# Performance work log

Hardware: AMD Instinct MI355X
Metric: run time of the kernel (lower is better)

The kernel has to match this reference:

```python
import jax, jax.numpy as jnp
import numpy as np

N, K, F = 16384, 64, 2048
ALPHA = 1.0
GAMMA = 1.0


def setup_inputs() -> dict:
    key = jax.random.key(0)
    k1, k2, k3, k4 = jax.random.split(key, 4)
    features = jax.random.normal(k1, (N, F), dtype=jnp.float32)
    idx = jax.random.randint(k2, (N,), 0, K)
    labels = jax.nn.one_hot(idx, K, dtype=jnp.float32)  # [N, K] one-hot
    # original initializes clusters to zeros (degenerate); use small random values
    cluster = jax.random.normal(k3, (K, F), dtype=jnp.float32) * 0.02
    class_weight = jax.random.uniform(k4, (K,), dtype=jnp.float32, minval=0.5, maxval=1.5)
    return {"features": features, "labels": labels, "cluster": cluster,
            "class_weight": class_weight}


def reference(features, labels, cluster, class_weight):
    # ci: cluster center of each sample's argmax label  [N, F]
    idx = jnp.argmax(labels, axis=1)
    ci = cluster[idx]
    # numerator: squared distance to own center  [N]
    nume = jnp.sum((features - ci) ** 2, axis=1)
    # denom: sum_j ||c_j - c_i||^2 + alpha  (TF flattens cj to [N, K*F] and
    # tiles ci K times; the squared norm over that axis is exactly this sum)
    d2 = jnp.sum((cluster[:, None, :] - cluster[None, :, :]) ** 2, axis=-1)  # [K, K]
    row_sum = jnp.sum(d2, axis=1)                                            # [K]
    denom = row_sum[idx] + ALPHA                                             # [N]
    loss = (nume / denom)[:, None]                                           # [N, 1]
    # cluster update: weighted_delta[k,f] = sum_n cw[n,k]*labels[n,k]*(x[n,f]-c[k,f])/denom[n]
    # with cw[n,k] = labels[n,k] * class_weight[k]. Expressed without the
    # [N,K,F] intermediates the TF code materializes:
    A = (labels * labels) * class_weight[None, :] / denom[:, None]  # [N, K]
    weighted_delta = jnp.einsum('nk,nf->kf', A, features) - jnp.sum(A, axis=0)[:, None] * cluster
    new_cluster = cluster - GAMMA * weighted_delta  # assign_sub side effect
    return loss, new_cluster
```

## Files before the change

### kernel.cpp

```cpp
#include <hip/hip_runtime.h>

#define NROWS 16384
#define KC 64
#define FDIM 2048
#define F4 (FDIM / 4)
#define ALPHA 1.0f
#define GAMMA 1.0f
#define ROWS 16
#define HB 128
#define ROWS_PER_HB 128

typedef float f32x4 __attribute__((ext_vector_type(4)));

__global__ __launch_bounds__(256) void k_argmax_hist(
    const float* __restrict__ labels, int* __restrict__ idx,
    int* __restrict__ blockHist, float4* __restrict__ delta4) {
    __shared__ int hist[KC];
    int t = threadIdx.x, w = t >> 6, lane = t & 63;
    if (t < KC) hist[t] = 0;
    float4 z = {0.f, 0.f, 0.f, 0.f};
    delta4[blockIdx.x * 256 + t] = z;
    __syncthreads();
    int rowbase = blockIdx.x * ROWS_PER_HB + w * 32;
    #pragma unroll
    for (int r0 = 0; r0 < 32; r0 += 4) {
        float v0 = labels[(rowbase + r0 + 0) * KC + lane];
        float v1 = labels[(rowbase + r0 + 1) * KC + lane];
        float v2 = labels[(rowbase + r0 + 2) * KC + lane];
        float v3 = labels[(rowbase + r0 + 3) * KC + lane];
        unsigned long long m0 = __ballot(v0 > 0.5f);
        unsigned long long m1 = __ballot(v1 > 0.5f);
        unsigned long long m2 = __ballot(v2 > 0.5f);
        unsigned long long m3 = __ballot(v3 > 0.5f);
        if (lane == 0) {
            int k0 = __ffsll(m0) - 1;
            int k1 = __ffsll(m1) - 1;
            int k2 = __ffsll(m2) - 1;
            int k3 = __ffsll(m3) - 1;
            idx[rowbase + r0 + 0] = k0;
            idx[rowbase + r0 + 1] = k1;
            idx[rowbase + r0 + 2] = k2;
            idx[rowbase + r0 + 3] = k3;
            atomicAdd(&hist[k0], 1);
            atomicAdd(&hist[k1], 1);
            atomicAdd(&hist[k2], 1);
            atomicAdd(&hist[k3], 1);
        }
    }
    __syncthreads();
    if (t < KC) blockHist[blockIdx.x * KC + t] = hist[t];
}

__global__ __launch_bounds__(256) void k_prefix_rowsum(
    const int* __restrict__ blockHist, int* __restrict__ blockBase,
    int* __restrict__ counts, int* __restrict__ offsets,
    const float* __restrict__ cluster, const float* __restrict__ cw,
    float* __restrict__ inv_denom, float* __restrict__ scale) {
    if (blockIdx.x == 0) {
        int t = threadIdx.x, c = t >> 6, k = t & 63;
        __shared__ int chunkTot[4][KC];
        __shared__ int kTot[KC];
        int acc = 0;
        for (int b = c * 32; b < c * 32 + 32; ++b) acc += blockHist[b * KC + k];
        chunkTot[c][k] = acc;
        __syncthreads();
        if (c == 0) {
            int tot = chunkTot[0][k] + chunkTot[1][k] + chunkTot[2][k] + chunkTot[3][k];
            kTot[k] = tot;
            counts[k] = tot;
        }
        __syncthreads();
        if (t == 0) {
            int a = 0;
            for (int j = 0; j < KC; ++j) { offsets[j] = a; a += kTot[j]; }
        }
        int run = 0;
        for (int cc = 0; cc < c; ++cc) run += chunkTot[cc][k];
        for (int b = c * 32; b < c * 32 + 32; ++b) {
            blockBase[b * KC + k] = run;
            run += blockHist[b * KC + k];
        }
    } else {
        int k = blockIdx.x - 1, t = threadIdx.x;
        const float4* c4 = (const float4*)cluster;
        float4 a0 = c4[k * F4 + t];
        float4 a1 = c4[k * F4 + 256 + t];
        float acc = 0.f;
        for (int j = 0; j < KC; ++j) {
            float4 b0 = c4[j * F4 + t];
            float4 b1 = c4[j * F4 + 256 + t];
            float d;
            d = a0.x - b0.x; acc += d * d;
            d = a0.y - b0.y; acc += d * d;
            d = a0.z - b0.z; acc += d * d;
            d = a0.w - b0.w; acc += d * d;
            d = a1.x - b1.x; acc += d * d;
            d = a1.y - b1.y; acc += d * d;
            d = a1.z - b1.z; acc += d * d;
            d = a1.w - b1.w; acc += d * d;
        }
        #pragma unroll
        for (int off = 32; off >= 1; off >>= 1) acc += __shfl_down(acc, off);
        __shared__ float red[4];
        if ((t & 63) == 0) red[t >> 6] = acc;
        __syncthreads();
        if (t == 0) {
            float denom = red[0] + red[1] + red[2] + red[3] + ALPHA;
            inv_denom[k] = 1.0f / denom;
            scale[k]     = cw[k] / denom;
        }
    }
}

__global__ __launch_bounds__(128) void k_scatter(
    const int* __restrict__ idx, const int* __restrict__ offsets,
    const int* __restrict__ blockBase, int* __restrict__ order) {
    __shared__ int cur[KC];
    int t = threadIdx.x;
    if (t < KC) cur[t] = offsets[t] + blockBase[blockIdx.x * KC + t];
    __syncthreads();
    int n = blockIdx.x * ROWS_PER_HB + t;
    int k = idx[n];
    int p = atomicAdd(&cur[k], 1);
    order[p] = n;
}

__global__ __launch_bounds__(256) void k_main(
    const float* __restrict__ features, const float* __restrict__ cluster,
    const int* __restrict__ idx, const int* __restrict__ order,
    const float* __restrict__ inv_denom, float* __restrict__ delta,
    float* __restrict__ lossPart) {
    int t = threadIdx.x;
    int pair = blockIdx.x >> 1, half = blockIdx.x & 1;
    int foff = half * 256;
    __shared__ float part[ROWS][256];
    __shared__ int onum[ROWS];
    __shared__ int okk[ROWS];
    if (t < ROWS) {
        int n = order[pair * ROWS + t];
        onum[t] = n;
        okk[t]  = idx[n];
    }
    __syncthreads();

    const f32x4* f4 = (const f32x4*)features;
    const f32x4* c4 = (const f32x4*)cluster;
    float4 s = {0.f, 0.f, 0.f, 0.f};
    int k0 = okk[0];

    if (okk[ROWS - 1] == k0) {
        f32x4 cv = c4[k0 * F4 + foff + t];
        for (int r = 0; r < ROWS; r += 4) {
            f32x4 x0 = __builtin_nontemporal_load(&f4[(size_t)onum[r + 0] * F4 + foff + t]);
            f32x4 x1 = __builtin_nontemporal_load(&f4[(size_t)onum[r + 1] * F4 + foff + t]);
            f32x4 x2 = __builtin_nontemporal_load(&f4[(size_t)onum[r + 2] * F4 + foff + t]);
            f32x4 x3 = __builtin_nontemporal_load(&f4[(size_t)onum[r + 3] * F4 + foff + t]);
            float d, p;
            s.x += x0.x; s.y += x0.y; s.z += x0.z; s.w += x0.w;
            p = 0.f;
            d = x0.x - cv.x; p += d * d;
            d = x0.y - cv.y; p += d * d;
            d = x0.z - cv.z; p += d * d;
            d = x0.w - cv.w; p += d * d;
            part[r + 0][t] = p;
            s.x += x1.x; s.y += x1.y; s.z += x1.z; s.w += x1.w;
            p = 0.f;
            d = x1.x - cv.x; p += d * d;
            d = x1.y - cv.y; p += d * d;
            d = x1.z - cv.z; p += d * d;
            d = x1.w - cv.w; p += d * d;
            part[r + 1][t] = p;
            s.x += x2.x; s.y += x2.y; s.z += x2.z; s.w += x2.w;
            p = 0.f;
            d = x2.x - cv.x; p += d * d;
            d = x2.y - cv.y; p += d * d;
            d = x2.z - cv.z; p += d * d;
            d = x2.w - cv.w; p += d * d;
            part[r + 2][t] = p;
            s.x += x3.x; s.y += x3.y; s.z += x3.z; s.w += x3.w;
            p = 0.f;
            d = x3.x - cv.x; p += d * d;
            d = x3.y - cv.y; p += d * d;
            d = x3.z - cv.z; p += d * d;
            d = x3.w - cv.w; p += d * d;
            part[r + 3][t] = p;
        }
        float* dk = delta + k0 * FDIM + half * 1024;
        atomicAdd(&dk[t * 4 + 0], s.x);
        atomicAdd(&dk[t * 4 + 1], s.y);
        atomicAdd(&dk[t * 4 + 2], s.z);
        atomicAdd(&dk[t * 4 + 3], s.w);
    } else {
        int cur_k = -1;
        f32x4 cv;
        for (int r = 0; r < ROWS; ++r) {
            int k = okk[r];
            if (k != cur_k) {
                if (cur_k >= 0) {
                    float* dk = delta + cur_k * FDIM + half * 1024;
                    atomicAdd(&dk[t * 4 + 0], s.x);
                    atomicAdd(&dk[t * 4 + 1], s.y);
                    atomicAdd(&dk[t * 4 + 2], s.z);
                    atomicAdd(&dk[t * 4 + 3], s.w);
                    s.x = s.y = s.z = s.w = 0.f;
                }
                cv = c4[k * F4 + foff + t];
                cur_k = k;
            }
            f32x4 x = __builtin_nontemporal_load(&f4[(size_t)onum[r] * F4 + foff + t]);
            s.x += x.x; s.y += x.y; s.z += x.z; s.w += x.w;
            float d, p = 0.f;
            d = x.x - cv.x; p += d * d;
            d = x.y - cv.y; p += d * d;
            d = x.z - cv.z; p += d * d;
            d = x.w - cv.w; p += d * d;
            part[r][t] = p;
        }
        float* dk = delta + cur_k * FDIM + half * 1024;
        atomicAdd(&dk[t * 4 + 0], s.x);
        atomicAdd(&dk[t * 4 + 1], s.y);
        atomicAdd(&dk[t * 4 + 2], s.z);
        atomicAdd(&dk[t * 4 + 3], s.w);
    }
    __syncthreads();
    int w = t >> 6, l = t & 63;
    for (int r = w; r < ROWS; r += 4) {
        float v = part[r][l] + part[r][l + 64] + part[r][l + 128] + part[r][l + 192];
        #pragma unroll
        for (int off = 32; off >= 1; off >>= 1) v += __shfl_down(v, off);
        if (l == 0) {
            lossPart[half * NROWS + onum[r]] = v * inv_denom[okk[r]];
        }
    }
}

__global__ __launch_bounds__(256) void k_finalize(
    const float* __restrict__ cluster, const float* __restrict__ delta,
    const int* __restrict__ counts, const float* __restrict__ scale,
    const float* __restrict__ lossPart, float* __restrict__ outc,
    float* __restrict__ loss) {
    int b = blockIdx.x, t = threadIdx.x;
    if (b < 128) {
        int e = b * 256 + t;
        int k = e >> 9;
        const float4* c4 = (const float4*)cluster;
        const float4* d4 = (const float4*)delta;
        float4 c = c4[e], d = d4[e];
        float s = scale[k], cnt = (float)counts[k];
        float4 o;
        o.x = c.x - GAMMA * s * (d.x - cnt * c.x);
        o.y = c.y - GAMMA * s * (d.y - cnt * c.y);
        o.z = c.z - GAMMA * s * (d.z - cnt * c.z);
        o.w = c.w - GAMMA * s * (d.w - cnt * c.w);
        ((float4*)outc)[e] = o;
    } else {
        int n = (b - 128) * 256 + t;
        loss[n] = lossPart[n] + lossPart[NROWS + n];
    }
}

extern "C" void kernel_launch(void* const* d_in, const int* in_sizes, int n_in,
                              void* d_out, int out_size, void* d_ws, size_t ws_size,
                              hipStream_t stream) {
    const float* features = (const float*)d_in[0];
    const float* labels   = (const float*)d_in[1];
    const float* cluster  = (const float*)d_in[2];
    const float* cw       = (const float*)d_in[3];
    float* loss = (float*)d_out;
    float* outc = (float*)d_out + NROWS;

    char*  ws        = (char*)d_ws;
    float* delta     = (float*)ws;
    int*   counts    = (int*)(ws + (size_t)KC * FDIM * 4);
    int*   offsets   = counts + KC;
    float* inv_denom = (float*)(offsets + KC);
    float* scale     = inv_denom + KC;
    int*   idx       = (int*)(scale + KC);
    int*   order     = idx + NROWS;
    int*   blockHist = order + NROWS;
    int*   blockBase = blockHist + HB * KC;
    float* lossPart  = (float*)(blockBase + HB * KC);

    k_argmax_hist<<<HB, 256, 0, stream>>>(labels, idx, blockHist, (float4*)delta);
    k_prefix_rowsum<<<KC + 1, 256, 0, stream>>>(blockHist, blockBase, counts, offsets,
                                                cluster, cw, inv_denom, scale);
    k_scatter<<<HB, 128, 0, stream>>>(idx, offsets, blockBase, order);
    k_main<<<(NROWS / ROWS) * 2, 256, 0, stream>>>(features, cluster, idx, order,
                                                   inv_denom, delta, lossPart);
    k_finalize<<<192, 256, 0, stream>>>(cluster, delta, counts, scale, lossPart,
                                        outc, loss);
}
```

Before: 225.2 us.

## Merge histogram, prefix and scatter into per-class sort kernel, widen main loads

```diff
diff --git a/kernel.cpp b/kernel.cpp
--- a/kernel.cpp
+++ b/kernel.cpp
@@ -7,21 +7,19 @@
 #define ALPHA 1.0f
 #define GAMMA 1.0f
 #define ROWS 16
-#define HB 128
-#define ROWS_PER_HB 128
+#define AB 128
+#define ROWS_PER_AB 128
+#define MAXCL 640
 
 typedef float f32x4 __attribute__((ext_vector_type(4)));
 
-__global__ __launch_bounds__(256) void k_argmax_hist(
+__global__ __launch_bounds__(256) void k_argmax(
     const float* __restrict__ labels, int* __restrict__ idx,
-    int* __restrict__ blockHist, float4* __restrict__ delta4) {
-    __shared__ int hist[KC];
+    float4* __restrict__ delta4) {
     int t = threadIdx.x, w = t >> 6, lane = t & 63;
-    if (t < KC) hist[t] = 0;
     float4 z = {0.f, 0.f, 0.f, 0.f};
     delta4[blockIdx.x * 256 + t] = z;
-    __syncthreads();
-    int rowbase = blockIdx.x * ROWS_PER_HB + w * 32;
+    int rowbase = blockIdx.x * ROWS_PER_AB + w * 32;
     #pragma unroll
     for (int r0 = 0; r0 < 32; r0 += 4) {
         float v0 = labels[(rowbase + r0 + 0) * KC + lane];
@@ -33,55 +31,45 @@
         unsigned long long m2 = __ballot(v2 > 0.5f);
         unsigned long long m3 = __ballot(v3 > 0.5f);
         if (lane == 0) {
-            int k0 = __ffsll(m0) - 1;
-            int k1 = __ffsll(m1) - 1;
-            int k2 = __ffsll(m2) - 1;
-            int k3 = __ffsll(m3) - 1;
-            idx[rowbase + r0 + 0] = k0;
-            idx[rowbase + r0 + 1] = k1;
-            idx[rowbase + r0 + 2] = k2;
-            idx[rowbase + r0 + 3] = k3;
-            atomicAdd(&hist[k0], 1);
-            atomicAdd(&hist[k1], 1);
-            atomicAdd(&hist[k2], 1);
-            atomicAdd(&hist[k3], 1);
-        }
-    }
-    __syncthreads();
-    if (t < KC) blockHist[blockIdx.x * KC + t] = hist[t];
-}
-
-__global__ __launch_bounds__(256) void k_prefix_rowsum(
-    const int* __restrict__ blockHist, int* __restrict__ blockBase,
-    int* __restrict__ counts, int* __restrict__ offsets,
+            idx[rowbase + r0 + 0] = __ffsll(m0) - 1;
+            idx[rowbase + r0 + 1] = __ffsll(m1) - 1;
+            idx[rowbase + r0 + 2] = __ffsll(m2) - 1;
+            idx[rowbase + r0 + 3] = __ffsll(m3) - 1;
+        }
+    }
+}
+
+__global__ __launch_bounds__(256) void k_sort_rowsum(
+    const int* __restrict__ idx, int* __restrict__ order,
+    int* __restrict__ counts,
     const float* __restrict__ cluster, const float* __restrict__ cw,
     float* __restrict__ inv_denom, float* __restrict__ scale) {
-    if (blockIdx.x == 0) {
-        int t = threadIdx.x, c = t >> 6, k = t & 63;
-        __shared__ int chunkTot[4][KC];
-        __shared__ int kTot[KC];
-        int acc = 0;
-        for (int b = c * 32; b < c * 32 + 32; ++b) acc += blockHist[b * KC + k];
-        chunkTot[c][k] = acc;
+    int t = threadIdx.x;
+    if (blockIdx.x < KC) {
+        int k = blockIdx.x;
+        __shared__ int list[MAXCL];
+        __shared__ int lcnt;
+        __shared__ int redv[4];
+        if (t == 0) lcnt = 0;
         __syncthreads();
-        if (c == 0) {
-            int tot = chunkTot[0][k] + chunkTot[1][k] + chunkTot[2][k] + chunkTot[3][k];
-            kTot[k] = tot;
-            counts[k] = tot;
-        }
+        int myless = 0;
+        #pragma unroll 4
+        for (int i = 0; i < NROWS / 256; ++i) {
+            int n = i * 256 + t;
+            int v = idx[n];
+            myless += (v < k) ? 1 : 0;
+            if (v == k) { int p = atomicAdd(&lcnt, 1); list[p] = n; }
+        }
+        #pragma unroll
+        for (int off = 32; off >= 1; off >>= 1) myless += __shfl_down(myless, off);
+        if ((t & 63) == 0) redv[t >> 6] = myless;
         __syncthreads();
-        if (t == 0) {
-            int a = 0;
-            for (int j = 0; j < KC; ++j) { offsets[j] = a; a += kTot[j]; }
-        }
-        int run = 0;
-        for (int cc = 0; cc < c; ++cc) run += chunkTot[cc][k];
-        for (int b = c * 32; b < c * 32 + 32; ++b) {
-            blockBase[b * KC + k] = run;
-            run += blockHist[b * KC + k];
-        }
+        int offk = redv[0] + redv[1] + redv[2] + redv[3];
+        int cnt = lcnt;
+        if (t == 0) counts[k] = cnt;
+        for (int i = t; i < cnt; i += 256) order[offk + i] = list[i];
     } else {
-        int k = blockIdx.x - 1, t = threadIdx.x;
+        int k = blockIdx.x - KC;
         const float4* c4 = (const float4*)cluster;
         float4 a0 = c4[k * F4 + t];
         float4 a1 = c4[k * F4 + 256 + t];
@@ -112,19 +100,6 @@
     }
 }
 
-__global__ __launch_bounds__(128) void k_scatter(
-    const int* __restrict__ idx, const int* __restrict__ offsets,
-    const int* __restrict__ blockBase, int* __restrict__ order) {
-    __shared__ int cur[KC];
-    int t = threadIdx.x;
-    if (t < KC) cur[t] = offsets[t] + blockBase[blockIdx.x * KC + t];
-    __syncthreads();
-    int n = blockIdx.x * ROWS_PER_HB + t;
-    int k = idx[n];
-    int p = atomicAdd(&cur[k], 1);
-    order[p] = n;
-}
-
 __global__ __launch_bounds__(256) void k_main(
     const float* __restrict__ features, const float* __restrict__ cluster,
     const int* __restrict__ idx, const int* __restrict__ order,
@@ -150,40 +125,21 @@
 
     if (okk[ROWS - 1] == k0) {
         f32x4 cv = c4[k0 * F4 + foff + t];
-        for (int r = 0; r < ROWS; r += 4) {
-            f32x4 x0 = __builtin_nontemporal_load(&f4[(size_t)onum[r + 0] * F4 + foff + t]);
-            f32x4 x1 = __builtin_nontemporal_load(&f4[(size_t)onum[r + 1] * F4 + foff + t]);
-            f32x4 x2 = __builtin_nontemporal_load(&f4[(size_t)onum[r + 2] * F4 + foff + t]);
-            f32x4 x3 = __builtin_nontemporal_load(&f4[(size_t)onum[r + 3] * F4 + foff + t]);
-            float d, p;
-            s.x += x0.x; s.y += x0.y; s.z += x0.z; s.w += x0.w;
-            p = 0.f;
-            d = x0.x - cv.x; p += d * d;
-            d = x0.y - cv.y; p += d * d;
-            d = x0.z - cv.z; p += d * d;
-            d = x0.w - cv.w; p += d * d;
-            part[r + 0][t] = p;
-            s.x += x1.x; s.y += x1.y; s.z += x1.z; s.w += x1.w;
-            p = 0.f;
-            d = x1.x - cv.x; p += d * d;
-            d = x1.y - cv.y; p += d * d;
-            d = x1.z - cv.z; p += d * d;
-            d = x1.w - cv.w; p += d * d;
-            part[r + 1][t] = p;
-            s.x += x2.x; s.y += x2.y; s.z += x2.z; s.w += x2.w;
-            p = 0.f;
-            d = x2.x - cv.x; p += d * d;
-            d = x2.y - cv.y; p += d * d;
-            d = x2.z - cv.z; p += d * d;
-            d = x2.w - cv.w; p += d * d;
-            part[r + 2][t] = p;
-            s.x += x3.x; s.y += x3.y; s.z += x3.z; s.w += x3.w;
-            p = 0.f;
-            d = x3.x - cv.x; p += d * d;
-            d = x3.y - cv.y; p += d * d;
-            d = x3.z - cv.z; p += d * d;
-            d = x3.w - cv.w; p += d * d;
-            part[r + 3][t] = p;
+        for (int r = 0; r < ROWS; r += 8) {
+            f32x4 x[8];
+            #pragma unroll
+            for (int j = 0; j < 8; ++j)
+                x[j] = __builtin_nontemporal_load(&f4[(size_t)onum[r + j] * F4 + foff + t]);
+            #pragma unroll
+            for (int j = 0; j < 8; ++j) {
+                s.x += x[j].x; s.y += x[j].y; s.z += x[j].z; s.w += x[j].w;
+                float d, p = 0.f;
+                d = x[j].x - cv.x; p += d * d;
+                d = x[j].y - cv.y; p += d * d;
+                d = x[j].z - cv.z; p += d * d;
+                d = x[j].w - cv.w; p += d * d;
+                part[r + j][t] = p;
+            }
         }
         float* dk = delta + k0 * FDIM + half * 1024;
         atomicAdd(&dk[t * 4 + 0], s.x);
@@ -272,19 +228,15 @@
     char*  ws        = (char*)d_ws;
     float* delta     = (float*)ws;
     int*   counts    = (int*)(ws + (size_t)KC * FDIM * 4);
-    int*   offsets   = counts + KC;
-    float* inv_denom = (float*)(offsets + KC);
+    float* inv_denom = (float*)(counts + KC);
     float* scale     = inv_denom + KC;
     int*   idx       = (int*)(scale + KC);
     int*   order     = idx + NROWS;
-    int*   blockHist = order + NROWS;
-    int*   blockBase = blockHist + HB * KC;
-    float* lossPart  = (float*)(blockBase + HB * KC);
-
-    k_argmax_hist<<<HB, 256, 0, stream>>>(labels, idx, blockHist, (float4*)delta);
-    k_prefix_rowsum<<<KC + 1, 256, 0, stream>>>(blockHist, blockBase, counts, offsets,
-                                                cluster, cw, inv_denom, scale);
-    k_scatter<<<HB, 128, 0, stream>>>(idx, offsets, blockBase, order);
+    float* lossPart  = (float*)(order + NROWS);
+
+    k_argmax<<<AB, 256, 0, stream>>>(labels, idx, (float4*)delta);
+    k_sort_rowsum<<<2 * KC, 256, 0, stream>>>(idx, order, counts,
+                                              cluster, cw, inv_denom, scale);
     k_main<<<(NROWS / ROWS) * 2, 256, 0, stream>>>(features, cluster, idx, order,
                                                    inv_denom, delta, lossPart);
     k_finalize<<<192, 256, 0, stream>>>(cluster, delta, counts, scale, lossPart,
```

Result: no change. 228.7 us (+1.5%).
